# Performance work log

Hardware: AMD Instinct MI355X
Metric: run time of the kernel (lower is better)

## Reference

```python
import jax, jax.numpy as jnp
import numpy as np

N = 50000
E = 800000
IN_DIM = 128
HID = 32
HEADS = 8
OUT_DIM = 64
BN_EPS = 1e-5
NEG_SLOPE = 0.2


def batch_norm(x, gamma, beta, mean, var):
    # eval-mode BatchNorm1d using running statistics
    return (x - mean) * jax.lax.rsqrt(var + BN_EPS) * gamma + beta


def gat_conv(x, src, dst, W, att_src, att_dst, heads, out_ch, n):
    """PyG GATConv (shared src/dst lin), self-loops already included in src/dst.
    x: [n, in]; W: [in, heads*out_ch]; att_*: [heads, out_ch].
    Returns [n, heads, out_ch]."""
    h = (x @ W).reshape(n, heads, out_ch)                       # node features per head
    a_s = jnp.einsum('nho,ho->nh', h, att_src)                  # [n, heads]
    a_d = jnp.einsum('nho,ho->nh', h, att_dst)
    e = jax.nn.leaky_relu(a_s[src] + a_d[dst], NEG_SLOPE)       # [e, heads]
    # segment softmax over incoming edges of each dst node
    mx = jax.ops.segment_max(e, dst, num_segments=n)
    ex = jnp.exp(e - mx[dst])
    denom = jax.ops.segment_sum(ex, dst, num_segments=n)
    alpha = ex / (denom[dst] + 1e-16)                           # [e, heads]
    out = jax.ops.segment_sum(alpha[:, :, None] * h[src], dst, num_segments=n)
    return out                                                  # [n, heads, out_ch]


def setup_inputs() -> dict:
    key = jax.random.key(0)
    ks = jax.random.split(key, 24)
    inp = {}
    inp['x'] = jax.random.normal(ks[0], (N, IN_DIM), dtype=jnp.float32)
    inp['edge_index'] = jax.random.randint(ks[1], (2, E), 0, N, dtype=jnp.int64)
    s = 0.05
    inp['W1'] = jax.random.normal(ks[2], (IN_DIM, HEADS * HID), dtype=jnp.float32) * s
    inp['a_src1'] = jax.random.normal(ks[3], (HEADS, HID), dtype=jnp.float32) * s
    inp['a_dst1'] = jax.random.normal(ks[4], (HEADS, HID), dtype=jnp.float32) * s
    inp['b1'] = jnp.zeros((HEADS * HID,), dtype=jnp.float32)
    inp['W2'] = jax.random.normal(ks[5], (HEADS * HID, OUT_DIM), dtype=jnp.float32) * s
    inp['a_src2'] = jax.random.normal(ks[6], (1, OUT_DIM), dtype=jnp.float32) * s
    inp['a_dst2'] = jax.random.normal(ks[7], (1, OUT_DIM), dtype=jnp.float32) * s
    inp['b2'] = jnp.zeros((OUT_DIM,), dtype=jnp.float32)
    # projection Linear(out_dim -> in_dim)
    inp['Wp'] = jax.random.normal(ks[8], (OUT_DIM, IN_DIM), dtype=jnp.float32) * s
    inp['bp'] = jnp.zeros((IN_DIM,), dtype=jnp.float32)
    # BatchNorm params (eval mode running stats)
    for i, d in [(1, HEADS * HID), (2, OUT_DIM), (3, IN_DIM)]:
        k0, k1, k2, k3 = jax.random.split(ks[8 + i], 4)
        inp[f'g{i}'] = 1.0 + 0.1 * jax.random.normal(k0, (d,), dtype=jnp.float32)
        inp[f'be{i}'] = 0.1 * jax.random.normal(k1, (d,), dtype=jnp.float32)
        inp[f'm{i}'] = 0.1 * jax.random.normal(k2, (d,), dtype=jnp.float32)
        inp[f'v{i}'] = jax.random.uniform(k3, (d,), dtype=jnp.float32, minval=0.5, maxval=1.5)
    return inp


def reference(x, edge_index, W1, a_src1, a_dst1, b1, W2, a_src2, a_dst2, b2,
              Wp, bp, g1, be1, m1, v1, g2, be2, m2, v2, g3, be3, m3, v3):
    n = x.shape[0]
    loops = jnp.arange(n, dtype=edge_index.dtype)
    src = jnp.concatenate([edge_index[0], loops])   # add_self_loops=True (PyG default)
    dst = jnp.concatenate([edge_index[1], loops])

    h = gat_conv(x, src, dst, W1, a_src1, a_dst1, HEADS, HID, n)
    h = h.reshape(n, HEADS * HID) + b1              # concat=True
    h = jax.nn.elu(batch_norm(h, g1, be1, m1, v1))  # dropout is no-op in eval

    h = gat_conv(h, src, dst, W2, a_src2, a_dst2, 1, OUT_DIM, n)
    h = h.reshape(n, OUT_DIM) + b2                  # concat=False, heads=1 -> mean == identity
    h = jax.nn.elu(batch_norm(h, g2, be2, m2, v2))

    h = h @ Wp + bp
    return batch_norm(h, g3, be3, m3, v3)
```

## Files before the change

### kernel.cpp

```cpp
#include <hip/hip_runtime.h>
#include <math.h>

#define NEG_SLOPE 0.2f
#define BN_EPS 1e-5f

typedef __bf16 bf16x8 __attribute__((ext_vector_type(8)));
typedef float  f32x4  __attribute__((ext_vector_type(4)));

__device__ __forceinline__ float elu_f(float x){ return x > 0.f ? x : expm1f(x); }
__device__ __forceinline__ float lrelu_f(float x){ return x > 0.f ? x : NEG_SLOPE * x; }

__device__ __forceinline__ float b2f(ushort u){
    union { uint i; float f; } v; v.i = (uint)u << 16; return v.f;
}
__device__ __forceinline__ ushort f2b(float f){
    union { float f; uint i; } v; v.f = f;
    uint r = v.i + 0x7FFFu + ((v.i >> 16) & 1u);
    return (ushort)(r >> 16);
}

__device__ __forceinline__ bool detect_f64(const void* ei, int E, long long N)
{
    const long long* p = (const long long*)ei;
    int lane = threadIdx.x & 63;
    long long v = p[lane % max(1, min(2 * E, 64))];
    bool bad = (v < 0 || v >= N);
    return __ballot(bad) == 0ull;
}

__device__ __forceinline__ void get_edge(const void* ei, int e, int E, bool f64, int& s, int& d)
{
    if (e < E) {
        if (f64) { const long long* p = (const long long*)ei; s = (int)p[e]; d = (int)p[E + e]; }
        else     { const int*       p = (const int*)ei;       s = p[e];      d = p[E + e]; }
    } else {
        s = d = e - E;
    }
}

__global__ void setup_kernel(const void* ei, int E, int N, int* deg, int cx,
    const float* __restrict__ x, ushort* __restrict__ xb,
    const float* __restrict__ W1, const float* __restrict__ W2, const float* __restrict__ Wp,
    ushort* __restrict__ wt1, ushort* __restrict__ wt2, ushort* __restrict__ wtp,
    const float* b1, const float* b2, const float* bp,
    const float* g1, const float* be1, const float* m1, const float* v1,
    const float* g2, const float* be2, const float* m2, const float* v2,
    const float* g3, const float* be3, const float* m3, const float* v3,
    float* par)
{
    int b = blockIdx.x, t = threadIdx.x;
    if (b == 0) {
        { float s = g1[t] * rsqrtf(v1[t] + BN_EPS); par[t] = s;        par[256 + t] = b1[t] * s + be1[t] - m1[t] * s; }
        if (t < 64)  { float s = g2[t] * rsqrtf(v2[t] + BN_EPS); par[512 + t] = s;  par[576 + t] = b2[t] * s + be2[t] - m2[t] * s; }
        if (t < 128) { float s = g3[t] * rsqrtf(v3[t] + BN_EPS); par[640 + t] = s;  par[768 + t] = bp[t] * s + be3[t] - m3[t] * s; }
    } else if (b <= 224) {
        int idx = (b - 1) * 256 + t;
        if (idx < 32768) {
            int n = idx >> 7, k = idx & 127;
            wt1[idx] = f2b(W1[k * 256 + n]);
        } else if (idx < 49152) {
            int j = idx - 32768;
            int n = j >> 8, k = j & 255;
            wt2[j] = f2b(W2[k * 64 + n]);
        } else if (idx < 57344) {
            int j = idx - 49152;
            int n = j >> 6, k = j & 63;
            wtp[j] = f2b(Wp[k * 128 + n]);
        }
    } else if (b < 225 + cx) {
        long long n128 = (long long)N * 128;
        long long idx = ((long long)(b - 225) * 256 + t) * 8;
        if (idx + 7 < n128) {
            float4 v0 = *reinterpret_cast<const float4*>(&x[idx]);
            float4 v1 = *reinterpret_cast<const float4*>(&x[idx + 4]);
            ushort o[8] = { f2b(v0.x), f2b(v0.y), f2b(v0.z), f2b(v0.w),
                            f2b(v1.x), f2b(v1.y), f2b(v1.z), f2b(v1.w) };
            uint4 pk;
            pk.x = (uint)o[0] | ((uint)o[1] << 16);
            pk.y = (uint)o[2] | ((uint)o[3] << 16);
            pk.z = (uint)o[4] | ((uint)o[5] << 16);
            pk.w = (uint)o[6] | ((uint)o[7] << 16);
            *reinterpret_cast<uint4*>(&xb[idx]) = pk;
        } else {
            for (long long q = idx; q < n128; ++q) xb[q] = f2b(x[q]);
        }
    } else {
        bool f64 = detect_f64(ei, E, (long long)N);
        int i = (b - 225 - cx) * 256 + t;
        int ET = E + N;
        if (i < ET) {
            int s, d;
            get_edge(ei, i, E, f64, s, d);
            atomicAdd(&deg[d], 1);
        }
    }
}

__global__ void scan1_kernel(const int* __restrict__ deg, int N, int* __restrict__ bsum)
{
    int b = blockIdx.x, t = threadIdx.x;
    int base = b * 4096 + t * 16;
    int s = 0;
    #pragma unroll
    for (int k = 0; k < 16; k += 4) {
        int idx = base + k;
        if (idx + 3 < N) {
            int4 v = *reinterpret_cast<const int4*>(&deg[idx]);
            s += v.x + v.y + v.z + v.w;
        } else {
            for (int q = 0; q < 4; ++q) if (idx + q < N) s += deg[idx + q];
        }
    }
    #pragma unroll
    for (int off = 1; off < 64; off <<= 1) s += __shfl_xor(s, off);
    __shared__ int wsum[4];
    if ((t & 63) == 0) wsum[t >> 6] = s;
    __syncthreads();
    if (t == 0) bsum[b] = wsum[0] + wsum[1] + wsum[2] + wsum[3];
}

__global__ void scan2_kernel(const int* __restrict__ bsum, int nb, int* __restrict__ bpre)
{
    if (threadIdx.x == 0) {
        int r = 0;
        for (int i = 0; i < nb; ++i) { bpre[i] = r; r += bsum[i]; }
        bpre[nb] = r;
    }
}

__global__ void scan3_kernel(const int* __restrict__ deg, int N,
                             const int* __restrict__ bpre, int nb,
                             int* __restrict__ rowptr, int* __restrict__ fillptr)
{
    int b = blockIdx.x, t = threadIdx.x;
    int base = b * 4096 + t * 16;
    int loc[16];
    int s = 0;
    #pragma unroll
    for (int k = 0; k < 16; ++k) {
        int idx = base + k;
        int d = (idx < N) ? deg[idx] : 0;
        loc[k] = s; s += d;
    }
    int lane = t & 63;
    int incl = s;
    #pragma unroll
    for (int off = 1; off < 64; off <<= 1) {
        int v = __shfl_up(incl, off);
        if (lane >= off) incl += v;
    }
    __shared__ int wsum[4];
    if (lane == 63) wsum[t >> 6] = incl;
    __syncthreads();
    int woff = 0;
    int w = t >> 6;
    for (int i = 0; i < w; ++i) woff += wsum[i];
    int off0 = bpre[b] + woff + incl - s;
    #pragma unroll
    for (int k = 0; k < 16; ++k) {
        int idx = base + k;
        if (idx < N) { rowptr[idx] = off0 + loc[k]; fillptr[idx] = off0 + loc[k]; }
    }
    if (b == 0 && t == 0) rowptr[N] = bpre[nb];
}

__global__ void fill_kernel(const void* ei, int E, int N, int* fillptr, int* esrc)
{
    bool f64 = detect_f64(ei, E, (long long)N);
    int i = blockIdx.x * blockDim.x + threadIdx.x;
    int ET = E + N;
    if (i >= ET) return;
    int s, d;
    get_edge(ei, i, E, f64, s, d);
    int pos = atomicAdd(&fillptr[d], 1);
    esrc[pos] = s;
}

template<int ATYPE, int OMODE, int ATT>
__global__ __launch_bounds__(256) void mgemm_kernel(const void* __restrict__ Ap,
    const ushort* __restrict__ Bt, void* __restrict__ Cp, int M, int K, int NC,
    const float* __restrict__ S, const float* __restrict__ Cc,
    const float* __restrict__ att_s, const float* __restrict__ att_d,
    float* __restrict__ as_out, float* __restrict__ ad_out)
{
    const int BM = 128, LDA = 72;
    __shared__ __align__(16) ushort As[BM][LDA];
    __shared__ __align__(16) ushort Bs[64][LDA];
    __shared__ float red[128][2];
    int t = threadIdx.x;
    int m0 = blockIdx.x * BM, n0 = blockIdx.y * 64;
    int w = t >> 6, l = t & 63;
    int wm = w >> 1, wn = w & 1;
    int r16 = l & 15, kg = l >> 4;

    f32x4 acc[4][2];
    #pragma unroll
    for (int mi = 0; mi < 4; ++mi)
        #pragma unroll
        for (int ni = 0; ni < 2; ++ni)
            acc[mi][ni] = (f32x4){0.f, 0.f, 0.f, 0.f};

    for (int kb = 0; kb < K; kb += 64) {
        if (ATYPE == 0) {
            const float* A = (const float*)Ap;
            #pragma unroll
            for (int p = 0; p < 8; ++p) {
                int r = (t >> 4) + p * 16, c4 = (t & 15) * 4;
                int gm = m0 + r;
                float4 v = (gm < M) ? *reinterpret_cast<const float4*>(&A[(size_t)gm * K + kb + c4])
                                    : make_float4(0.f, 0.f, 0.f, 0.f);
                ushort4 u; u.x = f2b(v.x); u.y = f2b(v.y); u.z = f2b(v.z); u.w = f2b(v.w);
                *reinterpret_cast<ushort4*>(&As[r][c4]) = u;
            }
        } else {
            const ushort* A = (const ushort*)Ap;
            #pragma unroll
            for (int p = 0; p < 4; ++p) {
                int r = (t >> 3) + p * 32, c8 = (t & 7) * 8;
                int gm = m0 + r;
                uint4 v = (gm < M) ? *reinterpret_cast<const uint4*>(&A[(size_t)gm * K + kb + c8])
                                   : make_uint4(0u, 0u, 0u, 0u);
                *reinterpret_cast<uint4*>(&As[r][c8]) = v;
            }
        }
        #pragma unroll
        for (int p = 0; p < 2; ++p) {
            int r = (t >> 3) + p * 32, c8 = (t & 7) * 8;
            uint4 v = *reinterpret_cast<const uint4*>(&Bt[(size_t)(n0 + r) * K + kb + c8]);
            *reinterpret_cast<uint4*>(&Bs[r][c8]) = v;
        }
        __syncthreads();
        #pragma unroll
        for (int kk = 0; kk < 2; ++kk) {
            bf16x8 bB[2], bA[4];
            #pragma unroll
            for (int ni = 0; ni < 2; ++ni)
                bB[ni] = *reinterpret_cast<const bf16x8*>(&Bs[wn * 32 + ni * 16 + r16][kk * 32 + kg * 8]);
            #pragma unroll
            for (int mi = 0; mi < 4; ++mi)
                bA[mi] = *reinterpret_cast<const bf16x8*>(&As[wm * 64 + mi * 16 + r16][kk * 32 + kg * 8]);
            #pragma unroll
            for (int mi = 0; mi < 4; ++mi)
                #pragma unroll
                for (int ni = 0; ni < 2; ++ni)
                    acc[mi][ni] = __builtin_amdgcn_mfma_f32_16x16x32_bf16(bA[mi], bB[ni], acc[mi][ni], 0, 0, 0);
        }
        __syncthreads();
    }
    #pragma unroll
    for (int mi = 0; mi < 4; ++mi) {
        #pragma unroll
        for (int ni = 0; ni < 2; ++ni) {
            #pragma unroll
            for (int rg = 0; rg < 4; ++rg) {
                int gm = m0 + wm * 64 + mi * 16 + kg * 4 + rg;
                int gc = n0 + wn * 32 + ni * 16 + r16;
                if (gm < M) {
                    float v = acc[mi][ni][rg];
                    if (OMODE == 0) ((ushort*)Cp)[(size_t)gm * NC + gc] = f2b(v);
                    else            ((float*)Cp)[(size_t)gm * NC + gc] = v * S[gc] + Cc[gc];
                }
            }
        }
    }
    if (ATT) {
        float cs0 = att_s[n0 + wn * 32 + r16], cs1 = att_s[n0 + wn * 32 + 16 + r16];
        float cd0 = att_d[n0 + wn * 32 + r16], cd1 = att_d[n0 + wn * 32 + 16 + r16];
        float sp[4][4], dp[4][4];
        #pragma unroll
        for (int mi = 0; mi < 4; ++mi)
            #pragma unroll
            for (int rg = 0; rg < 4; ++rg) {
                sp[mi][rg] = acc[mi][0][rg] * cs0 + acc[mi][1][rg] * cs1;
                dp[mi][rg] = acc[mi][0][rg] * cd0 + acc[mi][1][rg] * cd1;
            }
        #pragma unroll
        for (int off = 1; off < 16; off <<= 1)
            #pragma unroll
            for (int mi = 0; mi < 4; ++mi)
                #pragma unroll
                for (int rg = 0; rg < 4; ++rg) {
                    sp[mi][rg] += __shfl_xor(sp[mi][rg], off);
                    dp[mi][rg] += __shfl_xor(dp[mi][rg], off);
                }
        if (ATT == 1) {
            int head = (n0 >> 5) + wn;
            if (r16 == 0) {
                #pragma unroll
                for (int mi = 0; mi < 4; ++mi)
                    #pragma unroll
                    for (int rg = 0; rg < 4; ++rg) {
                        int gm = m0 + wm * 64 + mi * 16 + kg * 4 + rg;
                        if (gm < M) {
                            as_out[gm * 8 + head] = sp[mi][rg];
                            ad_out[gm * 8 + head] = dp[mi][rg];
                        }
                    }
            }
        } else {
            if (wn == 1 && r16 == 0) {
                #pragma unroll
                for (int mi = 0; mi < 4; ++mi)
                    #pragma unroll
                    for (int rg = 0; rg < 4; ++rg) {
                        int r = wm * 64 + mi * 16 + kg * 4 + rg;
                        red[r][0] = sp[mi][rg];
                        red[r][1] = dp[mi][rg];
                    }
            }
            __syncthreads();
            if (wn == 0 && r16 == 0) {
                #pragma unroll
                for (int mi = 0; mi < 4; ++mi)
                    #pragma unroll
                    for (int rg = 0; rg < 4; ++rg) {
                        int r = wm * 64 + mi * 16 + kg * 4 + rg;
                        int gm = m0 + r;
                        if (gm < M) {
                            as_out[gm] = sp[mi][rg] + red[r][0];
                            ad_out[gm] = dp[mi][rg] + red[r][1];
                        }
                    }
            }
        }
    }
}

__global__ void agg1_kernel(const ushort* __restrict__ h1,
                            const float* __restrict__ as1, const float* __restrict__ ad1,
                            const int* __restrict__ rowptr, const int* __restrict__ esrc,
                            const float* __restrict__ par,
                            ushort* __restrict__ outb, int N)
{
    __shared__ float wlds_all[4][64 * 8];
    __shared__ int   slds_all[4][64];
    float* wlds = wlds_all[threadIdx.x >> 6];
    int*   slds = slds_all[threadIdx.x >> 6];
    int wid = (blockIdx.x * blockDim.x + threadIdx.x) >> 6;
    int lane = threadIdx.x & 63;
    if (wid >= N) return;
    int beg = rowptr[wid], end = rowptr[wid + 1];
    int h = lane & 7, j = lane >> 3;
    int li = lane & 31, half = lane >> 5, hh = li >> 2;
    float ad_h = ad1[wid * 8 + h];
    float den = 0.f;
    float acc[8] = {0.f, 0.f, 0.f, 0.f, 0.f, 0.f, 0.f, 0.f};

    for (int cb = beg; cb < end; cb += 64) {
        int ce = min(cb + 64, end);
        for (int i = cb + j; i < ce; i += 8) {
            int src = esrc[i];
            float wv = __expf(lrelu_f(as1[src * 8 + h] + ad_h));
            wlds[(i - cb) * 8 + h] = wv;
            if (h == 0) slds[i - cb] = src;
            den += wv;
        }
        __builtin_amdgcn_wave_barrier();
        auto fma1 = [&](uint4 r, float al) {
            union { uint u; float f; } c0, c1;
            c0.u = r.x << 16; c1.u = r.x & 0xffff0000u; acc[0] += al * c0.f; acc[1] += al * c1.f;
            c0.u = r.y << 16; c1.u = r.y & 0xffff0000u; acc[2] += al * c0.f; acc[3] += al * c1.f;
            c0.u = r.z << 16; c1.u = r.z & 0xffff0000u; acc[4] += al * c0.f; acc[5] += al * c1.f;
            c0.u = r.w << 16; c1.u = r.w & 0xffff0000u; acc[6] += al * c0.f; acc[7] += al * c1.f;
        };
        int i = cb + half;
        for (; i + 14 < ce; i += 16) {
            uint4 r[8];
            #pragma unroll
            for (int q = 0; q < 8; ++q) {
                int src = slds[i + q * 2 - cb];
                r[q] = *reinterpret_cast<const uint4*>(&h1[(size_t)src * 256 + li * 8]);
            }
            #pragma unroll
            for (int q = 0; q < 8; ++q)
                fma1(r[q], wlds[(i + q * 2 - cb) * 8 + hh]);
        }
        for (; i < ce; i += 2) {
            int src = slds[i - cb];
            uint4 r = *reinterpret_cast<const uint4*>(&h1[(size_t)src * 256 + li * 8]);
            fma1(r, wlds[(i - cb) * 8 + hh]);
        }
        __builtin_amdgcn_wave_barrier();
    }

    den += __shfl_xor(den, 8, 64);
    den += __shfl_xor(den, 16, 64);
    den += __shfl_xor(den, 32, 64);
    float inv = 1.f / (den + 1e-16f);
    float inv_h = __shfl(inv, hh, 64);

    #pragma unroll
    for (int f = 0; f < 8; ++f) acc[f] += __shfl_xor(acc[f], 32, 64);
    if (half == 0) {
        int f0 = li * 8;
        const float* S1 = par;
        const float* C1 = par + 256;
        ushort o[8];
        #pragma unroll
        for (int f = 0; f < 8; ++f) o[f] = f2b(elu_f(acc[f] * inv_h * S1[f0 + f] + C1[f0 + f]));
        uint4 pk;
        pk.x = (uint)o[0] | ((uint)o[1] << 16);
        pk.y = (uint)o[2] | ((uint)o[3] << 16);
        pk.z = (uint)o[4] | ((uint)o[5] << 16);
        pk.w = (uint)o[6] | ((uint)o[7] << 16);
        *reinterpret_cast<uint4*>(&outb[(size_t)wid * 256 + f0]) = pk;
    }
}

__global__ void agg2_kernel(const ushort* __restrict__ h2,
                            const float* __restrict__ as2, const float* __restrict__ ad2,
                            const int* __restrict__ rowptr, const int* __restrict__ esrc,
                            const float* __restrict__ par,
                            ushort* __restrict__ outb, int N)
{
    __shared__ float wlds_all[4][64];
    __shared__ int   slds_all[4][64];
    float* wlds = wlds_all[threadIdx.x >> 6];
    int*   slds = slds_all[threadIdx.x >> 6];
    int wid = (blockIdx.x * blockDim.x + threadIdx.x) >> 6;
    int lane = threadIdx.x & 63;
    if (wid >= N) return;
    int beg = rowptr[wid], end = rowptr[wid + 1];
    int li = lane & 31, half = lane >> 5;
    float ad = ad2[wid];
    float den = 0.f;
    float a0 = 0.f, a1 = 0.f;

    for (int cb = beg; cb < end; cb += 64) {
        int ce = min(cb + 64, end);
        {
            int i = cb + lane;
            if (i < ce) {
                int src = esrc[i];
                float wv = __expf(lrelu_f(as2[src] + ad));
                wlds[i - cb] = wv;
                slds[i - cb] = src;
                den += wv;
            }
        }
        __builtin_amdgcn_wave_barrier();
        auto fma1 = [&](uint hv, float al) {
            union { uint u; float f; } c0, c1;
            c0.u = hv << 16; c1.u = hv & 0xffff0000u;
            a0 += al * c0.f; a1 += al * c1.f;
        };
        int i = cb + half;
        for (; i + 14 < ce; i += 16) {
            uint r[8];
            #pragma unroll
            for (int q = 0; q < 8; ++q) {
                int src = slds[i + q * 2 - cb];
                r[q] = *reinterpret_cast<const uint*>(&h2[(size_t)src * 64 + li * 2]);
            }
            #pragma unroll
            for (int q = 0; q < 8; ++q)
                fma1(r[q], wlds[i + q * 2 - cb]);
        }
        for (; i < ce; i += 2) {
            int src = slds[i - cb];
            uint r = *reinterpret_cast<const uint*>(&h2[(size_t)src * 64 + li * 2]);
            fma1(r, wlds[i - cb]);
        }
        __builtin_amdgcn_wave_barrier();
    }

    #pragma unroll
    for (int off = 1; off < 64; off <<= 1) den += __shfl_xor(den, off, 64);
    float inv = 1.f / (den + 1e-16f);
    a0 += __shfl_xor(a0, 32, 64);
    a1 += __shfl_xor(a1, 32, 64);
    if (half == 0) {
        int f = li * 2;
        const float* S2 = par + 512;
        const float* C2 = par + 576;
        ushort2 o;
        o.x = f2b(elu_f(a0 * inv * S2[f] + C2[f]));
        o.y = f2b(elu_f(a1 * inv * S2[f + 1] + C2[f + 1]));
        *reinterpret_cast<ushort2*>(&outb[(size_t)wid * 64 + f]) = o;
    }
}

extern "C" void kernel_launch(void* const* d_in, const int* in_sizes, int n_in,
                              void* d_out, int out_size, void* d_ws, size_t ws_size,
                              hipStream_t stream)
{
    const float* x      = (const float*)d_in[0];
    const void*  ei     = d_in[1];
    const float* W1     = (const float*)d_in[2];
    const float* a_src1 = (const float*)d_in[3];
    const float* a_dst1 = (const float*)d_in[4];
    const float* b1     = (const float*)d_in[5];
    const float* W2     = (const float*)d_in[6];
    const float* a_src2 = (const float*)d_in[7];
    const float* a_dst2 = (const float*)d_in[8];
    const float* b2     = (const float*)d_in[9];
    const float* Wp     = (const float*)d_in[10];
    const float* bp     = (const float*)d_in[11];
    const float* g1 = (const float*)d_in[12], *be1 = (const float*)d_in[13];
    const float* m1 = (const float*)d_in[14], *v1  = (const float*)d_in[15];
    const float* g2 = (const float*)d_in[16], *be2 = (const float*)d_in[17];
    const float* m2 = (const float*)d_in[18], *v2  = (const float*)d_in[19];
    const float* g3 = (const float*)d_in[20], *be3 = (const float*)d_in[21];
    const float* m3 = (const float*)d_in[22], *v3  = (const float*)d_in[23];
    float* out = (float*)d_out;

    const int N  = in_sizes[0] / 128;
    const int E  = in_sizes[1] / 2;
    const int ET = E + N;

    char* base = (char*)d_ws;
    size_t off = 0;
    auto alloc = [&](size_t bytes) -> char* {
        char* p = base + off;
        off += (bytes + 255) & ~(size_t)255;
        return p;
    };
    float*  par     = (float*)alloc(1024 * 4);
    int*    bsum    = (int*)alloc(256);
    int*    bpre    = (int*)alloc(256);
    int*    rowptr  = (int*)alloc((size_t)(N + 1) * 4);
    int*    fillptr = (int*)alloc((size_t)(N + 1) * 4);
    int*    esrc    = (int*)alloc((size_t)ET * 4);
    float*  as1     = (float*)alloc((size_t)N * 8 * 4);
    float*  ad1     = (float*)alloc((size_t)N * 8 * 4);
    float*  as2     = (float*)alloc((size_t)N * 4);
    float*  ad2     = (float*)alloc((size_t)N * 4);
    ushort* wt1     = (ushort*)alloc(256 * 128 * 2);
    ushort* wt2     = (ushort*)alloc(64 * 256 * 2);
    ushort* wtp     = (ushort*)alloc(128 * 64 * 2);
    ushort* xb      = (ushort*)alloc((size_t)N * 128 * 2);
    ushort* h1      = (ushort*)alloc((size_t)N * 256 * 2);
    ushort* h1b     = (ushort*)alloc((size_t)N * 256 * 2);
    ushort* h2      = (ushort*)alloc((size_t)N * 64 * 2);
    ushort* g2buf   = (ushort*)alloc((size_t)N * 64 * 2);

    hipMemsetAsync(fillptr, 0, (N + 1) * sizeof(int), stream);
    int cx = (int)(((size_t)N * 128 + 2047) / 2048);
    int cblocks = (ET + 255) / 256;
    setup_kernel<<<225 + cx + cblocks, 256, 0, stream>>>(ei, E, N, fillptr, cx,
        x, xb, W1, W2, Wp, wt1, wt2, wtp,
        b1, b2, bp, g1, be1, m1, v1, g2, be2, m2, v2, g3, be3, m3, v3, par);

    int nb = (N + 4095) / 4096;
    scan1_kernel<<<nb, 256, 0, stream>>>(fillptr, N, bsum);
    scan2_kernel<<<1, 64, 0, stream>>>(bsum, nb, bpre);
    scan3_kernel<<<nb, 256, 0, stream>>>(fillptr, N, bpre, nb, rowptr, fillptr);
    fill_kernel<<<cblocks, 256, 0, stream>>>(ei, E, N, fillptr, esrc);

    int mb128 = (N + 127) / 128;
    int wbl   = (N + 3) / 4;
    mgemm_kernel<1, 0, 1><<<dim3(mb128, 4), 256, 0, stream>>>(xb, wt1, h1, N, 128, 256,
        nullptr, nullptr, a_src1, a_dst1, as1, ad1);
    agg1_kernel<<<wbl, 256, 0, stream>>>(h1, as1, ad1, rowptr, esrc, par, h1b, N);

    mgemm_kernel<1, 0, 2><<<dim3(mb128, 1), 256, 0, stream>>>(h1b, wt2, h2, N, 256, 64,
        nullptr, nullptr, a_src2, a_dst2, as2, ad2);
    agg2_kernel<<<wbl, 256, 0, stream>>>(h2, as2, ad2, rowptr, esrc, par, g2buf, N);

    mgemm_kernel<1, 1, 0><<<dim3(mb128, 2), 256, 0, stream>>>(g2buf, wtp, out, N, 64, 128,
        par + 640, par + 768, nullptr, nullptr, nullptr, nullptr);
}
```

Measured before the change: 307.5 us.

## Split layer-1 aggregation across heads with one wave per node-head pair

The layer-1 aggregation kernel now assigns one wave to each (node, head) pair instead of one wave per node over all eight heads. Each lane loads 4-byte slices of the head's 32 features, and four edge groups are reduced with shuffles. This raises the wave count eightfold and shrinks per-wave LDS and registers, aiming at better occupancy and latency hiding. The cost is that each edge's source index and attention logit are read and recomputed once per head, and gathers become narrower. The layer-2 aggregation unroll is also cut from 8 to 4.

```diff
diff --git a/kernel.cpp b/kernel.cpp
--- a/kernel.cpp
+++ b/kernel.cpp
@@ -332,78 +332,72 @@
                             const float* __restrict__ par,
                             ushort* __restrict__ outb, int N)
 {
-    __shared__ float wlds_all[4][64 * 8];
+    __shared__ float wlds_all[4][64];
     __shared__ int   slds_all[4][64];
-    float* wlds = wlds_all[threadIdx.x >> 6];
-    int*   slds = slds_all[threadIdx.x >> 6];
-    int wid = (blockIdx.x * blockDim.x + threadIdx.x) >> 6;
+    int wslot = threadIdx.x >> 6;
+    float* wlds = wlds_all[wslot];
+    int*   slds = slds_all[wslot];
+    int s = blockIdx.x & 7;
+    int n = (blockIdx.x >> 3) * 4 + wslot;
     int lane = threadIdx.x & 63;
-    if (wid >= N) return;
-    int beg = rowptr[wid], end = rowptr[wid + 1];
-    int h = lane & 7, j = lane >> 3;
-    int li = lane & 31, half = lane >> 5, hh = li >> 2;
-    float ad_h = ad1[wid * 8 + h];
-    float den = 0.f;
-    float acc[8] = {0.f, 0.f, 0.f, 0.f, 0.f, 0.f, 0.f, 0.f};
+    if (n >= N) return;
+    int beg = rowptr[n], end = rowptr[n + 1];
+    float adv = ad1[n * 8 + s];
+    int q = lane >> 4, li = lane & 15;
+    int sf = s * 32;
+    float den = 0.f, a0 = 0.f, a1 = 0.f;
 
     for (int cb = beg; cb < end; cb += 64) {
         int ce = min(cb + 64, end);
-        for (int i = cb + j; i < ce; i += 8) {
+        int i = cb + lane;
+        if (i < ce) {
             int src = esrc[i];
-            float wv = __expf(lrelu_f(as1[src * 8 + h] + ad_h));
-            wlds[(i - cb) * 8 + h] = wv;
-            if (h == 0) slds[i - cb] = src;
+            float wv = __expf(lrelu_f(as1[src * 8 + s] + adv));
+            wlds[lane] = wv;
+            slds[lane] = src;
             den += wv;
         }
         __builtin_amdgcn_wave_barrier();
-        auto fma1 = [&](uint4 r, float al) {
+        int i2 = cb + q;
+        for (; i2 + 12 < ce; i2 += 16) {
+            uint r[4];
+            #pragma unroll
+            for (int k = 0; k < 4; ++k) {
+                int sr = slds[i2 + k * 4 - cb];
+                r[k] = *reinterpret_cast<const uint*>(&h1[(size_t)sr * 256 + sf + li * 2]);
+            }
+            #pragma unroll
+            for (int k = 0; k < 4; ++k) {
+                float al = wlds[i2 + k * 4 - cb];
+                union { uint u; float f; } c0, c1;
+                c0.u = r[k] << 16; c1.u = r[k] & 0xffff0000u;
+                a0 += al * c0.f; a1 += al * c1.f;
+            }
+        }
+        for (; i2 < ce; i2 += 4) {
+            int sr = slds[i2 - cb];
+            uint r = *reinterpret_cast<const uint*>(&h1[(size_t)sr * 256 + sf + li * 2]);
+            float al = wlds[i2 - cb];
             union { uint u; float f; } c0, c1;
-            c0.u = r.x << 16; c1.u = r.x & 0xffff0000u; acc[0] += al * c0.f; acc[1] += al * c1.f;
-            c0.u = r.y << 16; c1.u = r.y & 0xffff0000u; acc[2] += al * c0.f; acc[3] += al * c1.f;
-            c0.u = r.z << 16; c1.u = r.z & 0xffff0000u; acc[4] += al * c0.f; acc[5] += al * c1.f;
-            c0.u = r.w << 16; c1.u = r.w & 0xffff0000u; acc[6] += al * c0.f; acc[7] += al * c1.f;
-        };
-        int i = cb + half;
-        for (; i + 14 < ce; i += 16) {
-            uint4 r[8];
-            #pragma unroll
-            for (int q = 0; q < 8; ++q) {
-                int src = slds[i + q * 2 - cb];
-                r[q] = *reinterpret_cast<const uint4*>(&h1[(size_t)src * 256 + li * 8]);
-            }
-            #pragma unroll
-            for (int q = 0; q < 8; ++q)
-                fma1(r[q], wlds[(i + q * 2 - cb) * 8 + hh]);
-        }
-        for (; i < ce; i += 2) {
-            int src = slds[i - cb];
-            uint4 r = *reinterpret_cast<const uint4*>(&h1[(size_t)src * 256 + li * 8]);
-            fma1(r, wlds[(i - cb) * 8 + hh]);
+            c0.u = r << 16; c1.u = r & 0xffff0000u;
+            a0 += al * c0.f; a1 += al * c1.f;
         }
         __builtin_amdgcn_wave_barrier();
     }
 
-    den += __shfl_xor(den, 8, 64);
-    den += __shfl_xor(den, 16, 64);
-    den += __shfl_xor(den, 32, 64);
+    #pragma unroll
+    for (int off = 1; off < 64; off <<= 1) den += __shfl_xor(den, off, 64);
     float inv = 1.f / (den + 1e-16f);
-    float inv_h = __shfl(inv, hh, 64);
-
-    #pragma unroll
-    for (int f = 0; f < 8; ++f) acc[f] += __shfl_xor(acc[f], 32, 64);
-    if (half == 0) {
-        int f0 = li * 8;
+    a0 += __shfl_xor(a0, 16, 64); a0 += __shfl_xor(a0, 32, 64);
+    a1 += __shfl_xor(a1, 16, 64); a1 += __shfl_xor(a1, 32, 64);
+    if (lane < 16) {
+        int f = sf + li * 2;
         const float* S1 = par;
         const float* C1 = par + 256;
-        ushort o[8];
-        #pragma unroll
-        for (int f = 0; f < 8; ++f) o[f] = f2b(elu_f(acc[f] * inv_h * S1[f0 + f] + C1[f0 + f]));
-        uint4 pk;
-        pk.x = (uint)o[0] | ((uint)o[1] << 16);
-        pk.y = (uint)o[2] | ((uint)o[3] << 16);
-        pk.z = (uint)o[4] | ((uint)o[5] << 16);
-        pk.w = (uint)o[6] | ((uint)o[7] << 16);
-        *reinterpret_cast<uint4*>(&outb[(size_t)wid * 256 + f0]) = pk;
+        ushort2 o;
+        o.x = f2b(elu_f(a0 * inv * S1[f] + C1[f]));
+        o.y = f2b(elu_f(a1 * inv * S1[f + 1] + C1[f + 1]));
+        *reinterpret_cast<ushort2*>(&outb[(size_t)n * 256 + f]) = o;
     }
 }
 
@@ -445,16 +439,16 @@
             a0 += al * c0.f; a1 += al * c1.f;
         };
         int i = cb + half;
-        for (; i + 14 < ce; i += 16) {
-            uint r[8];
-            #pragma unroll
-            for (int q = 0; q < 8; ++q) {
-                int src = slds[i + q * 2 - cb];
-                r[q] = *reinterpret_cast<const uint*>(&h2[(size_t)src * 64 + li * 2]);
-            }
-            #pragma unroll
-            for (int q = 0; q < 8; ++q)
-                fma1(r[q], wlds[i + q * 2 - cb]);
+        for (; i + 6 < ce; i += 8) {
+            uint r[4];
+            #pragma unroll
+            for (int k = 0; k < 4; ++k) {
+                int src = slds[i + k * 2 - cb];
+                r[k] = *reinterpret_cast<const uint*>(&h2[(size_t)src * 64 + li * 2]);
+            }
+            #pragma unroll
+            for (int k = 0; k < 4; ++k)
+                fma1(r[k], wlds[i + k * 2 - cb]);
         }
         for (; i < ce; i += 2) {
             int src = slds[i - cb];
@@ -551,7 +545,7 @@
     int wbl   = (N + 3) / 4;
     mgemm_kernel<1, 0, 1><<<dim3(mb128, 4), 256, 0, stream>>>(xb, wt1, h1, N, 128, 256,
         nullptr, nullptr, a_src1, a_dst1, as1, ad1);
-    agg1_kernel<<<wbl, 256, 0, stream>>>(h1, as1, ad1, rowptr, esrc, par, h1b, N);
+    agg1_kernel<<<wbl * 8, 256, 0, stream>>>(h1, as1, ad1, rowptr, esrc, par, h1b, N);
 
     mgemm_kernel<1, 0, 2><<<dim3(mb128, 1), 256, 0, stream>>>(h1b, wt2, h2, N, 256, 64,
         nullptr, nullptr, a_src2, a_dst2, as2, ad2);
```

After: 387.3 us. 26.0% more time.
